# Kernel optimization log

Hardware: AMD Instinct MI355X
Metric: run time of the kernel (lower is better)

The kernel has to match this reference:

```python
import jax, jax.numpy as jnp
import numpy as np

N_NODES = 50000
N_EDGES = 800000
IN_FEATS, HIDDEN, OUT_FEATS = 512, 256, 128


def setup_inputs() -> dict:
    key = jax.random.key(0)
    ks = jax.random.split(key, 5)
    features = jax.random.normal(ks[0], (N_NODES, IN_FEATS), dtype=jnp.float32)
    W1 = jax.random.normal(ks[1], (IN_FEATS, HIDDEN), dtype=jnp.float32) * (1.0 / np.sqrt(IN_FEATS))
    b1 = jnp.zeros((HIDDEN,), dtype=jnp.float32)
    W2 = jax.random.normal(ks[2], (HIDDEN, OUT_FEATS), dtype=jnp.float32) * (1.0 / np.sqrt(HIDDEN))
    b2 = jnp.zeros((OUT_FEATS,), dtype=jnp.float32)
    src = jax.random.randint(ks[3], (N_EDGES,), 0, N_NODES, dtype=jnp.int32)
    dst = jax.random.randint(ks[4], (N_EDGES,), 0, N_NODES, dtype=jnp.int32)
    return {"features": features, "W1": W1, "b1": b1, "W2": W2, "b2": b2,
            "src": src, "dst": dst}


def reference(features, W1, b1, W2, b2, src, dst):
    # Two-layer GCN with DGL GraphConv norm='both':
    #   h = D_in^{-1/2} A D_out^{-1/2} (X W) + b
    N = features.shape[0]
    ones = jnp.ones(src.shape[0], dtype=features.dtype)
    deg_out = jnp.clip(jax.ops.segment_sum(ones, src, num_segments=N), 1.0)  # out-degree of src nodes
    deg_in = jnp.clip(jax.ops.segment_sum(ones, dst, num_segments=N), 1.0)   # in-degree of dst nodes
    norm_src = jax.lax.rsqrt(deg_out)[:, None]  # [N,1]
    norm_dst = jax.lax.rsqrt(deg_in)[:, None]   # [N,1]

    def gconv(x, W, b):
        h = (x * norm_src) @ W                                   # [N,d_out] weight first (in>out path)
        agg = jax.ops.segment_sum(h[src], dst, num_segments=N)   # sparse neighbor aggregation
        return agg * norm_dst + b

    h = jax.nn.relu(gconv(features, W1, b1))
    return gconv(h, W2, b2)
```

## Files before the change

### kernel.cpp

```cpp
#include <hip/hip_runtime.h>
#include <cstdint>
#include <cstddef>

#define NN 50000
#define NE 800000
static constexpr int IN_F = 512;
static constexpr int HID  = 256;
static constexpr int OUTF = 128;

typedef __attribute__((ext_vector_type(8))) _Float16 half8;
typedef __attribute__((ext_vector_type(4))) _Float16 half4v;
typedef __attribute__((ext_vector_type(2))) _Float16 half2v;
typedef __attribute__((ext_vector_type(4))) float f32x4;


__global__ void k_degree(const int* __restrict__ src, const int* __restrict__ dst,
                         int* __restrict__ deg_out, int* __restrict__ deg_in, int E) {
  int e = blockIdx.x * blockDim.x + threadIdx.x;
  if (e < E) {
    atomicAdd(&deg_out[src[e]], 1);
    atomicAdd(&deg_in[dst[e]], 1);
  }
}

__global__ void k_norm(const int* __restrict__ deg_out, const int* __restrict__ deg_in,
                       float* __restrict__ norm_src, float* __restrict__ norm_dst, int N) {
  int i = blockIdx.x * blockDim.x + threadIdx.x;
  if (i < N) {
    int dO = deg_out[i]; if (dO < 1) dO = 1;
    int dI = deg_in[i];  if (dI < 1) dI = 1;
    norm_src[i] = rsqrtf((float)dO);
    norm_dst[i] = rsqrtf((float)dI);
  }
}

__global__ void k_scan1(const int* __restrict__ deg_in, int* __restrict__ excl,
                        int* __restrict__ bsums, int N) {
  __shared__ int s[512];
  int t = threadIdx.x;
  int g = blockIdx.x * 512 + t;
  int v = (g < N) ? deg_in[g] : 0;
  s[t] = v;
  __syncthreads();
  for (int off = 1; off < 512; off <<= 1) {
    int add = (t >= off) ? s[t - off] : 0;
    __syncthreads();
    s[t] += add;
    __syncthreads();
  }
  if (g < N) excl[g] = s[t] - v;
  if (t == 511) bsums[blockIdx.x] = s[511];
}

__global__ void k_scan2(int* __restrict__ bsums, int nb) {
  __shared__ int s[128];
  int t = threadIdx.x;
  int v = (t < nb) ? bsums[t] : 0;
  s[t] = v;
  __syncthreads();
  for (int off = 1; off < 128; off <<= 1) {
    int add = (t >= off) ? s[t - off] : 0;
    __syncthreads();
    s[t] += add;
    __syncthreads();
  }
  if (t < nb) bsums[t] = s[t] - v;
}

__global__ void k_scan3(int* __restrict__ row_off, const int* __restrict__ bsums,
                        int N, int E) {
  int g = blockIdx.x * blockDim.x + threadIdx.x;
  if (g < N) row_off[g] += bsums[g >> 9];
  if (g == 0) row_off[N] = E;
}

__global__ void k_fill(const int* __restrict__ src, const int* __restrict__ dst,
                       const int* __restrict__ row_off, int* __restrict__ cursor,
                       int* __restrict__ ssrc, int E) {
  int e = blockIdx.x * blockDim.x + threadIdx.x;
  if (e < E) {
    int d = dst[e];
    int pos = atomicAdd(&cursor[d], 1);
    ssrc[row_off[d] + pos] = src[e];
  }
}

__global__ void k_convW(const float* __restrict__ W, _Float16* __restrict__ WT,
                        int K, int N) {
  int t = blockIdx.x * blockDim.x + threadIdx.x;
  if (t >= K * N) return;
  int n = t / K, k = t - n * K;
  WT[t] = (_Float16)W[(size_t)k * N + n];
}

template <bool AF32, bool SCALE>
__launch_bounds__(256, 6)
__global__ void k_gemm_f16(const void* __restrict__ Ap,
                           const _Float16* __restrict__ BT,
                           const float* __restrict__ rowscale,
                           _Float16* __restrict__ C, int M, int N, int K) {
  __shared__ uint4 sA[2][256];
  __shared__ uint4 sB[2][512];

  const int tid = threadIdx.x;
  const int wid = tid >> 6, lane = tid & 63;
  const int bm = blockIdx.x * 64, bn = blockIdx.y * 128;
  const int wrow = wid >> 1, wcol = wid & 1;

  const _Float16* Af16 = (const _Float16*)Ap;
  const float* Af32 = (const float*)Ap;

  const float* pa = nullptr;
  float sc = 1.f;
  if constexpr (AF32) {
    const int f = tid >> 6, r = tid & 63;
    int g = bm + f * 16 + (r & 15); if (g > M - 1) g = M - 1;
    if constexpr (SCALE) sc = rowscale[g];
    pa = Af32 + (size_t)g * K + (r >> 4) * 8;
  }

  float4 av0, av1;
  auto loadA32 = [&](int k0) {
    av0 = *(const float4*)(pa + k0);
    av1 = *(const float4*)(pa + k0 + 4);
  };
  auto cvtWriteA = [&](int buf) {
    float fv[8] = {av0.x, av0.y, av0.z, av0.w, av1.x, av1.y, av1.z, av1.w};
    union { _Float16 h[8]; uint4 q; } pk;
#pragma unroll
    for (int i = 0; i < 8; ++i)
      pk.h[i] = (_Float16)(SCALE ? fv[i] * sc : fv[i]);
    sA[buf][tid] = pk.q;
  };
  auto stageA16 = [&](int buf, int k0) {
    const int f = wid;
    int g = bm + f * 16 + (lane & 15); if (g > M - 1) g = M - 1;
    const _Float16* s = Af16 + (size_t)g * K + k0 + (lane >> 4) * 8;
    __builtin_amdgcn_global_load_lds(
        (const __attribute__((address_space(1))) unsigned int*)s,
        (__attribute__((address_space(3))) unsigned int*)&sA[buf][f * 64], 16, 0, 0);
  };
  auto stageB = [&](int buf, int k0) {
#pragma unroll
    for (int i = 0; i < 2; ++i) {
      const int f = wid * 2 + i;
      const _Float16* s = BT + (size_t)(bn + f * 16 + (lane & 15)) * K + k0 + (lane >> 4) * 8;
      __builtin_amdgcn_global_load_lds(
          (const __attribute__((address_space(1))) unsigned int*)s,
          (__attribute__((address_space(3))) unsigned int*)&sB[buf][f * 64], 16, 0, 0);
    }
  };

  f32x4 acc[2][4] = {};
  auto mfmaPhase = [&](int buf) {
    half8 ah[2], bh[4];
#pragma unroll
    for (int m = 0; m < 2; ++m)
      ah[m] = *(const half8*)&sA[buf][(wrow * 2 + m) * 64 + lane];
#pragma unroll
    for (int n = 0; n < 4; ++n)
      bh[n] = *(const half8*)&sB[buf][(wcol * 4 + n) * 64 + lane];
#pragma unroll
    for (int m = 0; m < 2; ++m)
#pragma unroll
      for (int n = 0; n < 4; ++n)
        acc[m][n] = __builtin_amdgcn_mfma_f32_16x16x32_f16(ah[m], bh[n], acc[m][n], 0, 0, 0);
  };

  const int nt = K >> 5;
  if constexpr (AF32) loadA32(0); else stageA16(0, 0);
  stageB(0, 0);
  if constexpr (AF32) cvtWriteA(0);
  __syncthreads();
  for (int t = 0; t < nt; ++t) {
    const int cur = t & 1;
    const bool more = (t + 1 < nt);
    if (more) {
      if constexpr (AF32) loadA32((t + 1) << 5); else stageA16(cur ^ 1, (t + 1) << 5);
      stageB(cur ^ 1, (t + 1) << 5);
    }
    mfmaPhase(cur);
    if (more) { if constexpr (AF32) cvtWriteA(cur ^ 1); }
    __syncthreads();
  }

#pragma unroll
  for (int m = 0; m < 2; ++m) {
    const int rb = bm + wrow * 32 + m * 16 + (lane >> 4) * 4;
#pragma unroll
    for (int r = 0; r < 4; ++r) {
      const int gm = rb + r;
      if (gm < M) {
        _Float16* cp = C + (size_t)gm * N + bn + wcol * 64 + (lane & 15);
#pragma unroll
        for (int n = 0; n < 4; ++n) cp[n * 16] = (_Float16)acc[m][n][r];
      }
    }
  }
}

template <int F, bool RELU, bool OSCALE, bool OUT16>
__launch_bounds__(256)
__global__ void k_agg16(const _Float16* __restrict__ H, const int* __restrict__ row_off,
                        const int* __restrict__ ssrc, const float* __restrict__ norm_dst,
                        const float* __restrict__ bias, const float* __restrict__ oscale,
                        void* __restrict__ outp, int N) {
  int wid = (blockIdx.x * 256 + threadIdx.x) >> 6;
  int lane = threadIdx.x & 63;
  if (wid >= N) return;
  int beg = row_off[wid], end = row_off[wid + 1];
  float nd = norm_dst[wid];

  if constexpr (F == 256) {
    float a0[4] = {}, a1[4] = {}, a2[4] = {}, a3[4] = {};
    int e = beg;
    for (; e + 4 <= end; e += 4) {
      int s0 = ssrc[e], s1 = ssrc[e + 1], s2 = ssrc[e + 2], s3 = ssrc[e + 3];
      half4v v0 = *(const half4v*)(H + (size_t)s0 * 256 + lane * 4);
      half4v v1 = *(const half4v*)(H + (size_t)s1 * 256 + lane * 4);
      half4v v2 = *(const half4v*)(H + (size_t)s2 * 256 + lane * 4);
      half4v v3 = *(const half4v*)(H + (size_t)s3 * 256 + lane * 4);
#pragma unroll
      for (int i = 0; i < 4; ++i) {
        a0[i] += (float)v0[i]; a1[i] += (float)v1[i];
        a2[i] += (float)v2[i]; a3[i] += (float)v3[i];
      }
    }
    for (; e < end; ++e) {
      half4v v = *(const half4v*)(H + (size_t)ssrc[e] * 256 + lane * 4);
#pragma unroll
      for (int i = 0; i < 4; ++i) a0[i] += (float)v[i];
    }
    const float4 bb = *(const float4*)(bias + lane * 4);
    float bv[4] = {bb.x, bb.y, bb.z, bb.w};
    float o[4];
#pragma unroll
    for (int i = 0; i < 4; ++i) {
      o[i] = fmaf(a0[i] + a1[i] + a2[i] + a3[i], nd, bv[i]);
      if (RELU) o[i] = fmaxf(o[i], 0.f);
    }
    if (OSCALE) {
      float os = oscale[wid];
#pragma unroll
      for (int i = 0; i < 4; ++i) o[i] *= os;
    }
    if constexpr (OUT16) {
      union { _Float16 h[4]; uint2 q; } pk;
#pragma unroll
      for (int i = 0; i < 4; ++i) pk.h[i] = (_Float16)o[i];
      *(uint2*)((_Float16*)outp + (size_t)wid * 256 + lane * 4) = pk.q;
    } else {
      *(float4*)((float*)outp + (size_t)wid * 256 + lane * 4) =
          make_float4(o[0], o[1], o[2], o[3]);
    }
  } else {
    float a0[2] = {}, a1[2] = {}, a2[2] = {}, a3[2] = {};
    int e = beg;
    for (; e + 4 <= end; e += 4) {
      int s0 = ssrc[e], s1 = ssrc[e + 1], s2 = ssrc[e + 2], s3 = ssrc[e + 3];
      half2v v0 = *(const half2v*)(H + (size_t)s0 * 128 + lane * 2);
      half2v v1 = *(const half2v*)(H + (size_t)s1 * 128 + lane * 2);
      half2v v2 = *(const half2v*)(H + (size_t)s2 * 128 + lane * 2);
      half2v v3 = *(const half2v*)(H + (size_t)s3 * 128 + lane * 2);
#pragma unroll
      for (int i = 0; i < 2; ++i) {
        a0[i] += (float)v0[i]; a1[i] += (float)v1[i];
        a2[i] += (float)v2[i]; a3[i] += (float)v3[i];
      }
    }
    for (; e < end; ++e) {
      half2v v = *(const half2v*)(H + (size_t)ssrc[e] * 128 + lane * 2);
#pragma unroll
      for (int i = 0; i < 2; ++i) a0[i] += (float)v[i];
    }
    const float2 bb = *(const float2*)(bias + lane * 2);
    float bv[2] = {bb.x, bb.y};
    float o[2];
#pragma unroll
    for (int i = 0; i < 2; ++i) {
      o[i] = fmaf(a0[i] + a1[i] + a2[i] + a3[i], nd, bv[i]);
      if (RELU) o[i] = fmaxf(o[i], 0.f);
    }
    if (OSCALE) {
      float os = oscale[wid];
#pragma unroll
      for (int i = 0; i < 2; ++i) o[i] *= os;
    }
    if constexpr (OUT16) {
      union { _Float16 h[2]; unsigned q; } pk;
      pk.h[0] = (_Float16)o[0]; pk.h[1] = (_Float16)o[1];
      *(unsigned*)((_Float16*)outp + (size_t)wid * 128 + lane * 2) = pk.q;
    } else {
      *(float2*)((float*)outp + (size_t)wid * 128 + lane * 2) = make_float2(o[0], o[1]);
    }
  }
}


extern "C" void kernel_launch(void* const* d_in, const int* in_sizes, int n_in,
                              void* d_out, int out_size, void* d_ws, size_t ws_size,
                              hipStream_t stream) {
  const float* X  = (const float*)d_in[0];
  const float* W1 = (const float*)d_in[1];
  const float* b1 = (const float*)d_in[2];
  const float* W2 = (const float*)d_in[3];
  const float* b2 = (const float*)d_in[4];
  const int* src  = (const int*)d_in[5];
  const int* dst  = (const int*)d_in[6];
  float* out = (float*)d_out;

  char* p = (char*)d_ws;
  auto alloc = [&](size_t bytes) -> char* {
    char* r = p;
    p += (bytes + 255) & ~(size_t)255;
    return r;
  };
  _Float16* H1pre  = (_Float16*)alloc((size_t)NN * HID * 2);
  _Float16* H1post = (_Float16*)alloc((size_t)NN * HID * 2);
  _Float16* H2pre  = H1pre;
  _Float16* W1T = (_Float16*)alloc((size_t)HID * IN_F * 2);
  _Float16* W2T = (_Float16*)alloc((size_t)OUTF * HID * 2);
  int* deg_out  = (int*)alloc((size_t)NN * 4);
  int* deg_in   = (int*)alloc((size_t)NN * 4);
  int* cursor   = (int*)alloc((size_t)NN * 4);
  int* row_off  = (int*)alloc((size_t)(NN + 1) * 4);
  int* bsums    = (int*)alloc(512);
  float* nsrc   = (float*)alloc((size_t)NN * 4);
  float* ndst   = (float*)alloc((size_t)NN * 4);
  int* ssrc     = (int*)alloc((size_t)NE * 4);

  hipMemsetAsync(deg_out, 0, (size_t)((char*)row_off - (char*)deg_out), stream);

  k_degree<<<(NE + 255) / 256, 256, 0, stream>>>(src, dst, deg_out, deg_in, NE);
  k_norm<<<(NN + 255) / 256, 256, 0, stream>>>(deg_out, deg_in, nsrc, ndst, NN);

  int nb = (NN + 511) / 512;
  k_scan1<<<nb, 512, 0, stream>>>(deg_in, row_off, bsums, NN);
  k_scan2<<<1, 128, 0, stream>>>(bsums, nb);
  k_scan3<<<(NN + 255) / 256, 256, 0, stream>>>(row_off, bsums, NN, NE);
  k_fill<<<(NE + 255) / 256, 256, 0, stream>>>(src, dst, row_off, cursor, ssrc, NE);

  k_convW<<<(IN_F * HID + 255) / 256, 256, 0, stream>>>(W1, W1T, IN_F, HID);
  k_convW<<<(HID * OUTF + 255) / 256, 256, 0, stream>>>(W2, W2T, HID, OUTF);

  dim3 g1((NN + 63) / 64, HID / 128);
  k_gemm_f16<true, true><<<g1, 256, 0, stream>>>(X, W1T, nsrc, H1pre, NN, HID, IN_F);
  k_agg16<256, true, true, true><<<(NN * 64 + 255) / 256, 256, 0, stream>>>(
      H1pre, row_off, ssrc, ndst, b1, nsrc, H1post, NN);

  dim3 g2((NN + 63) / 64, OUTF / 128);
  k_gemm_f16<false, false><<<g2, 256, 0, stream>>>(H1post, W2T, nullptr, H2pre, NN, OUTF, HID);
  k_agg16<128, false, false, false><<<(NN * 64 + 255) / 256, 256, 0, stream>>>(
      H2pre, row_off, ssrc, ndst, b2, nullptr, out, NN);
}
```

Measured before the change: 429.5 us.

## Keep full-K weight tile resident in LDS and stream A directly to registers

Replaces the double-buffered GEMM with a kernel that loads the whole K-extent of a 64-column weight slice into LDS once, then has each wave stream its own A rows straight from global memory into registers, prefetching two k-steps ahead. This removes the per-k-step LDS staging of A and the barrier inside the k-loop. Block tiles change to 128x64 with launch bounds tuned per layer. Costs are larger LDS use (64 KB for layer 1), which limits occupancy, and A fragments are now loaded directly by each wave with no sharing through LDS.

```diff
diff --git a/kernel.cpp b/kernel.cpp
--- a/kernel.cpp
+++ b/kernel.cpp
@@ -93,105 +93,119 @@
   WT[t] = (_Float16)W[(size_t)k * N + n];
 }
 
-template <bool AF32, bool SCALE>
-__launch_bounds__(256, 6)
-__global__ void k_gemm_f16(const void* __restrict__ Ap,
-                           const _Float16* __restrict__ BT,
-                           const float* __restrict__ rowscale,
-                           _Float16* __restrict__ C, int M, int N, int K) {
-  __shared__ uint4 sA[2][256];
-  __shared__ uint4 sB[2][512];
+template <bool AF32, bool SCALE, int NT, int LB>
+__launch_bounds__(256, LB)
+__global__ void k_gemm_bres(const void* __restrict__ Ap,
+                            const _Float16* __restrict__ BT,
+                            const float* __restrict__ rowscale,
+                            _Float16* __restrict__ C, int M, int N) {
+  constexpr int K = NT * 32;
+  __shared__ uint4 sB[4 * NT * 64];
 
   const int tid = threadIdx.x;
   const int wid = tid >> 6, lane = tid & 63;
-  const int bm = blockIdx.x * 64, bn = blockIdx.y * 128;
-  const int wrow = wid >> 1, wcol = wid & 1;
-
+  const int bm = blockIdx.x * 128, bn = blockIdx.y * 64;
+
+  {
+    const _Float16* base =
+        BT + (size_t)(bn + wid * 16 + (lane & 15)) * K + (lane >> 4) * 8;
+#pragma unroll
+    for (int ks = 0; ks < NT; ++ks) {
+      __builtin_amdgcn_global_load_lds(
+          (const __attribute__((address_space(1))) unsigned int*)(base + ks * 32),
+          (__attribute__((address_space(3))) unsigned int*)&sB[(wid * NT + ks) * 64 + lane],
+          16, 0, 0);
+    }
+  }
+
+  int r0 = bm + wid * 32 + (lane & 15);
+  int r1 = r0 + 16;
+  if (r0 > M - 1) r0 = M - 1;
+  if (r1 > M - 1) r1 = M - 1;
+  const float* Af32 = (const float*)Ap;
   const _Float16* Af16 = (const _Float16*)Ap;
-  const float* Af32 = (const float*)Ap;
-
-  const float* pa = nullptr;
-  float sc = 1.f;
+  float s0 = 1.f, s1 = 1.f;
+  const float *paf0 = nullptr, *paf1 = nullptr;
+  const _Float16 *pah0 = nullptr, *pah1 = nullptr;
   if constexpr (AF32) {
-    const int f = tid >> 6, r = tid & 63;
-    int g = bm + f * 16 + (r & 15); if (g > M - 1) g = M - 1;
-    if constexpr (SCALE) sc = rowscale[g];
-    pa = Af32 + (size_t)g * K + (r >> 4) * 8;
-  }
-
-  float4 av0, av1;
-  auto loadA32 = [&](int k0) {
-    av0 = *(const float4*)(pa + k0);
-    av1 = *(const float4*)(pa + k0 + 4);
+    if constexpr (SCALE) { s0 = rowscale[r0]; s1 = rowscale[r1]; }
+    paf0 = Af32 + (size_t)r0 * K + (lane >> 4) * 8;
+    paf1 = Af32 + (size_t)r1 * K + (lane >> 4) * 8;
+  } else {
+    pah0 = Af16 + (size_t)r0 * K + (lane >> 4) * 8;
+    pah1 = Af16 + (size_t)r1 * K + (lane >> 4) * 8;
+  }
+
+  float4 aL[2][2], aH[2][2];
+  uint4 aq[2][2];
+
+  auto loadA = [&](int ks, int slot) {
+    if constexpr (AF32) {
+      aL[slot][0] = *(const float4*)(paf0 + ks * 32);
+      aH[slot][0] = *(const float4*)(paf0 + ks * 32 + 4);
+      aL[slot][1] = *(const float4*)(paf1 + ks * 32);
+      aH[slot][1] = *(const float4*)(paf1 + ks * 32 + 4);
+    } else {
+      aq[slot][0] = *(const uint4*)(pah0 + ks * 32);
+      aq[slot][1] = *(const uint4*)(pah1 + ks * 32);
+    }
   };
-  auto cvtWriteA = [&](int buf) {
-    float fv[8] = {av0.x, av0.y, av0.z, av0.w, av1.x, av1.y, av1.z, av1.w};
-    union { _Float16 h[8]; uint4 q; } pk;
-#pragma unroll
-    for (int i = 0; i < 8; ++i)
-      pk.h[i] = (_Float16)(SCALE ? fv[i] * sc : fv[i]);
-    sA[buf][tid] = pk.q;
-  };
-  auto stageA16 = [&](int buf, int k0) {
-    const int f = wid;
-    int g = bm + f * 16 + (lane & 15); if (g > M - 1) g = M - 1;
-    const _Float16* s = Af16 + (size_t)g * K + k0 + (lane >> 4) * 8;
-    __builtin_amdgcn_global_load_lds(
-        (const __attribute__((address_space(1))) unsigned int*)s,
-        (__attribute__((address_space(3))) unsigned int*)&sA[buf][f * 64], 16, 0, 0);
-  };
-  auto stageB = [&](int buf, int k0) {
-#pragma unroll
-    for (int i = 0; i < 2; ++i) {
-      const int f = wid * 2 + i;
-      const _Float16* s = BT + (size_t)(bn + f * 16 + (lane & 15)) * K + k0 + (lane >> 4) * 8;
-      __builtin_amdgcn_global_load_lds(
-          (const __attribute__((address_space(1))) unsigned int*)s,
-          (__attribute__((address_space(3))) unsigned int*)&sB[buf][f * 64], 16, 0, 0);
-    }
-  };
 
   f32x4 acc[2][4] = {};
-  auto mfmaPhase = [&](int buf) {
-    half8 ah[2], bh[4];
-#pragma unroll
-    for (int m = 0; m < 2; ++m)
-      ah[m] = *(const half8*)&sA[buf][(wrow * 2 + m) * 64 + lane];
-#pragma unroll
-    for (int n = 0; n < 4; ++n)
-      bh[n] = *(const half8*)&sB[buf][(wcol * 4 + n) * 64 + lane];
-#pragma unroll
-    for (int m = 0; m < 2; ++m)
-#pragma unroll
-      for (int n = 0; n < 4; ++n)
-        acc[m][n] = __builtin_amdgcn_mfma_f32_16x16x32_f16(ah[m], bh[n], acc[m][n], 0, 0, 0);
-  };
-
-  const int nt = K >> 5;
-  if constexpr (AF32) loadA32(0); else stageA16(0, 0);
-  stageB(0, 0);
-  if constexpr (AF32) cvtWriteA(0);
+
+  loadA(0, 0);
+  if constexpr (NT > 1) loadA(1, 1);
   __syncthreads();
-  for (int t = 0; t < nt; ++t) {
-    const int cur = t & 1;
-    const bool more = (t + 1 < nt);
-    if (more) {
-      if constexpr (AF32) loadA32((t + 1) << 5); else stageA16(cur ^ 1, (t + 1) << 5);
-      stageB(cur ^ 1, (t + 1) << 5);
-    }
-    mfmaPhase(cur);
-    if (more) { if constexpr (AF32) cvtWriteA(cur ^ 1); }
-    __syncthreads();
+
+#pragma unroll
+  for (int ks = 0; ks < NT; ++ks) {
+    const int slot = ks & 1;
+    half8 af0, af1;
+    if constexpr (AF32) {
+      const float4 l0 = aL[slot][0], h0 = aH[slot][0];
+      const float4 l1 = aL[slot][1], h1 = aH[slot][1];
+      if constexpr (SCALE) {
+        af0[0]=(_Float16)(l0.x*s0); af0[1]=(_Float16)(l0.y*s0);
+        af0[2]=(_Float16)(l0.z*s0); af0[3]=(_Float16)(l0.w*s0);
+        af0[4]=(_Float16)(h0.x*s0); af0[5]=(_Float16)(h0.y*s0);
+        af0[6]=(_Float16)(h0.z*s0); af0[7]=(_Float16)(h0.w*s0);
+        af1[0]=(_Float16)(l1.x*s1); af1[1]=(_Float16)(l1.y*s1);
+        af1[2]=(_Float16)(l1.z*s1); af1[3]=(_Float16)(l1.w*s1);
+        af1[4]=(_Float16)(h1.x*s1); af1[5]=(_Float16)(h1.y*s1);
+        af1[6]=(_Float16)(h1.z*s1); af1[7]=(_Float16)(h1.w*s1);
+      } else {
+        af0[0]=(_Float16)l0.x; af0[1]=(_Float16)l0.y;
+        af0[2]=(_Float16)l0.z; af0[3]=(_Float16)l0.w;
+        af0[4]=(_Float16)h0.x; af0[5]=(_Float16)h0.y;
+        af0[6]=(_Float16)h0.z; af0[7]=(_Float16)h0.w;
+        af1[0]=(_Float16)l1.x; af1[1]=(_Float16)l1.y;
+        af1[2]=(_Float16)l1.z; af1[3]=(_Float16)l1.w;
+        af1[4]=(_Float16)h1.x; af1[5]=(_Float16)h1.y;
+        af1[6]=(_Float16)h1.z; af1[7]=(_Float16)h1.w;
+      }
+    } else {
+      union { uint4 q; half8 h; } u0, u1;
+      u0.q = aq[slot][0]; u1.q = aq[slot][1];
+      af0 = u0.h; af1 = u1.h;
+    }
+    if (ks + 2 < NT) loadA(ks + 2, slot);
+#pragma unroll
+    for (int nf = 0; nf < 4; ++nf) {
+      union { uint4 q; half8 h; } ub;
+      ub.q = sB[(nf * NT + ks) * 64 + lane];
+      acc[0][nf] = __builtin_amdgcn_mfma_f32_16x16x32_f16(af0, ub.h, acc[0][nf], 0, 0, 0);
+      acc[1][nf] = __builtin_amdgcn_mfma_f32_16x16x32_f16(af1, ub.h, acc[1][nf], 0, 0, 0);
+    }
   }
 
 #pragma unroll
   for (int m = 0; m < 2; ++m) {
-    const int rb = bm + wrow * 32 + m * 16 + (lane >> 4) * 4;
+    const int rb = bm + wid * 32 + m * 16 + (lane >> 4) * 4;
 #pragma unroll
     for (int r = 0; r < 4; ++r) {
       const int gm = rb + r;
       if (gm < M) {
-        _Float16* cp = C + (size_t)gm * N + bn + wcol * 64 + (lane & 15);
+        _Float16* cp = C + (size_t)gm * N + bn + (lane & 15);
 #pragma unroll
         for (int n = 0; n < 4; ++n) cp[n * 16] = (_Float16)acc[m][n][r];
       }
@@ -343,13 +357,15 @@
   k_convW<<<(IN_F * HID + 255) / 256, 256, 0, stream>>>(W1, W1T, IN_F, HID);
   k_convW<<<(HID * OUTF + 255) / 256, 256, 0, stream>>>(W2, W2T, HID, OUTF);
 
-  dim3 g1((NN + 63) / 64, HID / 128);
-  k_gemm_f16<true, true><<<g1, 256, 0, stream>>>(X, W1T, nsrc, H1pre, NN, HID, IN_F);
+  dim3 g1((NN + 127) / 128, HID / 64);
+  k_gemm_bres<true, true, IN_F / 32, 2><<<g1, 256, 0, stream>>>(
+      X, W1T, nsrc, H1pre, NN, HID);
   k_agg16<256, true, true, true><<<(NN * 64 + 255) / 256, 256, 0, stream>>>(
       H1pre, row_off, ssrc, ndst, b1, nsrc, H1post, NN);
 
-  dim3 g2((NN + 63) / 64, OUTF / 128);
-  k_gemm_f16<false, false><<<g2, 256, 0, stream>>>(H1post, W2T, nullptr, H2pre, NN, OUTF, HID);
+  dim3 g2((NN + 127) / 128, OUTF / 64);
+  k_gemm_bres<false, false, HID / 32, 4><<<g2, 256, 0, stream>>>(
+      H1post, W2T, nullptr, H2pre, NN, OUTF);
   k_agg16<128, false, false, false><<<(NN * 64 + 255) / 256, 256, 0, stream>>>(
       H2pre, row_off, ssrc, ndst, b2, nullptr, out, NN);
 }
```

Result: slower. 454.7 us (+5.9%).
